# Kernel tuning notes

Measured on AMD Instinct MI355X. Metric: run time of the kernel, lower is better.

## Reference

```python
import jax, jax.numpy as jnp
import numpy as np

H = 12          # heads in the ViT blocks
D = 768         # model dim (hard-coded in the module)
DFF = 3072      # mlp hidden = 4*D
ADIM = 64       # adapter bottleneck dim
L = 32          # num_latents
EPS = 1e-6      # timm ViT LayerNorm eps


def _ln(x, g, b):
    m = jnp.mean(x, axis=-1, keepdims=True)
    v = jnp.var(x, axis=-1, keepdims=True)
    return (x - m) * jax.lax.rsqrt(v + EPS) * g + b


def _quick_gelu(x):
    return x * jax.nn.sigmoid(1.702 * x)


def _sh_attn(q, k, v):
    # single-head attention used by fusion(); scale = C**-0.5 with C = full dim
    C = q.shape[-1]
    a = jax.nn.softmax(jnp.einsum('bnc,bmc->bnm', q, k) * (C ** -0.5), axis=-1)
    return jnp.einsum('bnm,bmc->bnc', a, v)


def _mhsa(x, qkv_w, qkv_b, proj_w, proj_b):
    B, N, C = x.shape
    Dh = C // H
    qkv = (x @ qkv_w.T + qkv_b).reshape(B, N, 3, H, Dh).transpose(2, 0, 3, 1, 4)
    q, k, v = qkv[0], qkv[1], qkv[2]                       # [B,H,N,Dh]
    a = jax.nn.softmax(jnp.einsum('bhnd,bhmd->bhnm', q, k) * (Dh ** -0.5), axis=-1)
    o = jnp.einsum('bhnm,bhmd->bhnd', a, v).transpose(0, 2, 1, 3).reshape(B, N, C)
    return o @ proj_w.T + proj_b


def _stream(t, ln1_g, ln1_b, qkv_w, qkv_b, proj_w, proj_b,
            ln2_g, ln2_b, fc1_w, fc1_b, fc2_w, fc2_b,
            down_w, down_b, up_w, up_b, scale):
    t = t + _mhsa(_ln(t, ln1_g, ln1_b), qkv_w, qkv_b, proj_w, proj_b)
    h = _ln(t, ln2_g, ln2_b)
    mlp = jax.nn.gelu(h @ fc1_w.T + fc1_b, approximate=False) @ fc2_w.T + fc2_b
    adapter = (_quick_gelu(h @ down_w.T + down_b) @ up_w.T + up_b) * scale
    return t + mlp + adapter


def setup_inputs() -> dict:
    key = jax.random.key(0)
    ks = iter(jax.random.split(key, 64))
    f32 = jnp.float32
    def rn(shape, std=0.02):
        return (jax.random.normal(next(ks), shape, dtype=f32) * std)
    inp = {
        'x': jax.random.normal(next(ks), (16, 512, 768), dtype=f32),
        'y': jax.random.normal(next(ks), (16, 196, 768), dtype=f32),
        'latents': rn((1, L, D)),
        'scale_a': jnp.full((1,), 0.5, f32),
        'scale_v': jnp.full((1,), 0.5, f32),
    }
    for p in ('spec', 'rgb'):
        inp.update({
            f'{p}_ln1_g': jnp.ones((D,), f32), f'{p}_ln1_b': jnp.zeros((D,), f32),
            f'{p}_qkv_w': rn((3 * D, D)), f'{p}_qkv_b': jnp.zeros((3 * D,), f32),
            f'{p}_proj_w': rn((D, D)), f'{p}_proj_b': jnp.zeros((D,), f32),
            f'{p}_ln2_g': jnp.ones((D,), f32), f'{p}_ln2_b': jnp.zeros((D,), f32),
            f'{p}_fc1_w': rn((DFF, D)), f'{p}_fc1_b': jnp.zeros((DFF,), f32),
            f'{p}_fc2_w': rn((D, DFF)), f'{p}_fc2_b': jnp.zeros((D,), f32),
            f'{p}_down_w': rn((ADIM, D)), f'{p}_down_b': jnp.zeros((ADIM,), f32),
            f'{p}_up_w': rn((D, ADIM)), f'{p}_up_b': jnp.zeros((D,), f32),
            f'{p}_scale': jnp.ones((1,), f32),
        })
    return inp


def reference(x, y, latents, scale_a, scale_v,
              spec_ln1_g, spec_ln1_b, spec_qkv_w, spec_qkv_b, spec_proj_w, spec_proj_b,
              spec_ln2_g, spec_ln2_b, spec_fc1_w, spec_fc1_b, spec_fc2_w, spec_fc2_b,
              spec_down_w, spec_down_b, spec_up_w, spec_up_b, spec_scale,
              rgb_ln1_g, rgb_ln1_b, rgb_qkv_w, rgb_qkv_b, rgb_proj_w, rgb_proj_b,
              rgb_ln2_g, rgb_ln2_b, rgb_fc1_w, rgb_fc1_b, rgb_fc2_w, rgb_fc2_b,
              rgb_down_w, rgb_down_b, rgb_up_w, rgb_up_b, rgb_scale):
    B = x.shape[0]
    # --- fusion via latent bottleneck (single-head attention) ---
    concat_ = jnp.concatenate((x, y), axis=1)                 # [B, Na+Nv, D]
    lat = jnp.broadcast_to(latents, (B, L, D))
    fused = _sh_attn(lat, concat_, concat_)                   # [B, L, D]
    x = x + scale_a * _sh_attn(x, fused, fused)
    y = y + scale_v * _sh_attn(y, fused, fused)
    # --- per-stream transformer block + adapter (dropout = eval/identity) ---
    x = _stream(x, spec_ln1_g, spec_ln1_b, spec_qkv_w, spec_qkv_b, spec_proj_w, spec_proj_b,
                spec_ln2_g, spec_ln2_b, spec_fc1_w, spec_fc1_b, spec_fc2_w, spec_fc2_b,
                spec_down_w, spec_down_b, spec_up_w, spec_up_b, spec_scale)
    y = _stream(y, rgb_ln1_g, rgb_ln1_b, rgb_qkv_w, rgb_qkv_b, rgb_proj_w, rgb_proj_b,
                rgb_ln2_g, rgb_ln2_b, rgb_fc1_w, rgb_fc1_b, rgb_fc2_w, rgb_fc2_b,
                rgb_down_w, rgb_down_b, rgb_up_w, rgb_up_b, rgb_scale)
    return (x, y)
```

## Files before the change

kernel.cpp:

```cpp
#include <hip/hip_runtime.h>
#include <hip/hip_bf16.h>


#define H_HEADS 12
#define DMODEL 768
#define DFF 3072
#define ADIM 64
#define NLAT 32
#define BATCH 16
#define NA 512
#define NV 196
#define NTOT 708
#define MCAT (BATCH * NTOT)

typedef __hip_bfloat16 bf16;
using bf16x8 = __attribute__((ext_vector_type(8))) short;
using f32x4  = __attribute__((ext_vector_type(4))) float;

static __device__ __forceinline__ float bf2f(bf16 v) { return __bfloat162float(v); }
static __device__ __forceinline__ float bflo(unsigned u) { return __uint_as_float(u << 16); }
static __device__ __forceinline__ float ld1(const float* p) { return *p; }
static __device__ __forceinline__ float ld1(const bf16* p) { return bf2f(*p); }
static __device__ __forceinline__ unsigned short f2bf_bits(float v) {
    unsigned u = __float_as_uint(v);
    return (unsigned short)((u + 0x7fffu + ((u >> 16) & 1u)) >> 16);
}

#define GLD_LDS16(gp, lp) __builtin_amdgcn_global_load_lds( \
    (const __attribute__((address_space(1))) void*)(gp), \
    (__attribute__((address_space(3))) void*)(lp), 16, 0, 0)

__global__ void detect_dtype_kernel(const unsigned short* __restrict__ x, int* __restrict__ flag)
{
    if (threadIdx.x == 0 && blockIdx.x == 0) {
        int big = 0;
        for (int i = 0; i < 2048; i++) {
            unsigned e = (x[i] >> 7) & 0xFF;
            if (e >= 0x90) big++;
        }
        flag[0] = (big > 16) ? 1 : 0;
        flag[1] = 0;
    }
}

template<typename TIn>
static __device__ __forceinline__ void pack_body(
    const TIn* __restrict__ x, const TIn* __restrict__ y, const TIn* __restrict__ lat,
    bf16* __restrict__ Cc, bf16* __restrict__ Lb)
{
    const int r = blockIdx.x, tid = threadIdx.x;
    const TIn* src;
    bf16* dst;
    if (r < MCAT) {
        const int b = r / NTOT, n = r - b * NTOT;
        src = (n < NA) ? x + ((size_t)(b * NA + n)) * DMODEL
                       : y + ((size_t)(b * NV + (n - NA))) * DMODEL;
        dst = Cc + (size_t)r * DMODEL;
    } else {
        src = lat + (size_t)(r - MCAT) * DMODEL;
        dst = Lb + (size_t)(r - MCAT) * DMODEL;
    }
    dst[tid]       = __float2bfloat16(ld1(src + tid));
    dst[tid + 256] = __float2bfloat16(ld1(src + tid + 256));
    dst[tid + 512] = __float2bfloat16(ld1(src + tid + 512));
}

__global__ __launch_bounds__(256)
void pack_concat_kernel(const int* __restrict__ flag, const void* x, const void* y,
                        const void* lat, bf16* __restrict__ Cc, bf16* __restrict__ Lb)
{
    if (flag[0]) pack_body<float>((const float*)x, (const float*)y, (const float*)lat, Cc, Lb);
    else         pack_body<bf16>((const bf16*)x, (const bf16*)y, (const bf16*)lat, Cc, Lb);
}

__global__ __launch_bounds__(64)
void fusion_softmax_kernel(const float* __restrict__ scores, float* __restrict__ P)
{
    const int b = blockIdx.x >> 5, l = blockIdx.x & 31, lane = threadIdx.x;
    const float* sp = scores + (size_t)b * NTOT * NLAT + l;
    float v[12];
    float mx = -1e30f;
    #pragma unroll
    for (int i = 0; i < 12; i++) {
        const int n = lane + i * 64;
        v[i] = (n < NTOT) ? sp[(size_t)n * NLAT] * 0.03608439182435161f : -1e30f;
        mx = fmaxf(mx, v[i]);
    }
    #pragma unroll
    for (int off = 32; off; off >>= 1) mx = fmaxf(mx, __shfl_xor(mx, off));
    float den = 0.f;
    #pragma unroll
    for (int i = 0; i < 12; i++) { v[i] = __expf(v[i] - mx); den += v[i]; }
    #pragma unroll
    for (int off = 32; off; off >>= 1) den += __shfl_xor(den, off);
    const float inv = 1.0f / den;
    float* op = P + ((size_t)b * NLAT + l) * 768;
    #pragma unroll
    for (int i = 0; i < 12; i++) {
        const int n = lane + i * 64;
        op[n] = (n < NTOT) ? v[i] * inv : 0.f;
    }
}

__global__ __launch_bounds__(256)
void fusion_wsum_kernel(const bf16* __restrict__ Cc, const float* __restrict__ P,
                        bf16* __restrict__ fused)
{
    const int b = blockIdx.y, d0 = blockIdx.x * 128;
    const int tid = threadIdx.x;
    const int lg = tid >> 5, dg = tid & 31;
    const int l0 = lg * 4;

    __shared__ float Ct[64][132];
    __shared__ float Ps[32][68];

    float acc[4][4] = {};

    for (int nc = 0; nc < 12; nc++) {
        const int n0 = nc * 64;
        __syncthreads();
        #pragma unroll
        for (int it = 0; it < 8; it++) {
            const int idx = it * 1024 + tid * 4;
            const int r = idx >> 7, c = idx & 127;
            const int gn = n0 + r;
            float4 v = make_float4(0.f, 0.f, 0.f, 0.f);
            if (gn < NTOT) {
                const ushort4 u = *(const ushort4*)(Cc + ((size_t)(b * NTOT + gn)) * DMODEL + d0 + c);
                v = make_float4(bflo(u.x), bflo(u.y), bflo(u.z), bflo(u.w));
            }
            Ct[r][c] = v.x; Ct[r][c + 1] = v.y; Ct[r][c + 2] = v.z; Ct[r][c + 3] = v.w;
        }
        {
            const int l = tid >> 3, off = (tid & 7) * 8;
            const float* pp = P + ((size_t)b * NLAT + l) * 768 + n0 + off;
            const float4 p0 = *(const float4*)pp;
            const float4 p1 = *(const float4*)(pp + 4);
            Ps[l][off] = p0.x; Ps[l][off + 1] = p0.y; Ps[l][off + 2] = p0.z; Ps[l][off + 3] = p0.w;
            Ps[l][off + 4] = p1.x; Ps[l][off + 5] = p1.y; Ps[l][off + 6] = p1.z; Ps[l][off + 7] = p1.w;
        }
        __syncthreads();

        for (int n = 0; n < 64; n++) {
            const float4 v = *(const float4*)&Ct[n][dg * 4];
            #pragma unroll
            for (int i = 0; i < 4; i++) {
                const float p = Ps[l0 + i][n];
                acc[i][0] += p * v.x; acc[i][1] += p * v.y;
                acc[i][2] += p * v.z; acc[i][3] += p * v.w;
            }
        }
    }

    #pragma unroll
    for (int i = 0; i < 4; i++) {
        bf16* op = fused + ((size_t)b * NLAT + l0 + i) * DMODEL + d0 + dg * 4;
        #pragma unroll
        for (int j = 0; j < 4; j++) op[j] = __float2bfloat16(acc[i][j]);
    }
}

template<typename TIn>
static __device__ __forceinline__ void attend_fused_body(
    const TIn* __restrict__ t, const bf16* __restrict__ fused,
    const TIn* __restrict__ scale_p, bf16* __restrict__ out, int Npb)
{
    const int tid = threadIdx.x;
    const int gid = blockIdx.x;
    const int b = gid / Npb;
    const TIn* row = t + (size_t)gid * DMODEL;
    const bf16* fb = fused + (size_t)b * NLAT * DMODEL;

    __shared__ float q[DMODEL];
    __shared__ float p[NLAT];

    for (int d = tid; d < DMODEL; d += 256) q[d] = ld1(row + d);
    __syncthreads();

    const int g = tid >> 3, li = tid & 7;
    float s = 0.f;
    const bf16* fr = fb + (size_t)g * DMODEL;
    for (int d = li; d < DMODEL; d += 8) s += q[d] * bf2f(fr[d]);
    s += __shfl_xor(s, 1); s += __shfl_xor(s, 2); s += __shfl_xor(s, 4);
    if (li == 0) p[g] = s * 0.03608439182435161f;
    __syncthreads();

    float mx = -1e30f;
    #pragma unroll
    for (int l = 0; l < NLAT; l++) mx = fmaxf(mx, p[l]);
    float w[NLAT];
    float den = 0.f;
    #pragma unroll
    for (int l = 0; l < NLAT; l++) { w[l] = __expf(p[l] - mx); den += w[l]; }
    const float sA = ld1(scale_p) / den;

    float a0 = 0.f, a1 = 0.f, a2 = 0.f;
    #pragma unroll
    for (int l = 0; l < NLAT; l++) {
        const bf16* fv = fb + (size_t)l * DMODEL;
        a0 += w[l] * bf2f(fv[tid]);
        a1 += w[l] * bf2f(fv[tid + 256]);
        a2 += w[l] * bf2f(fv[tid + 512]);
    }
    bf16* o = out + (size_t)gid * DMODEL;
    o[tid]       = __float2bfloat16(q[tid]       + sA * a0);
    o[tid + 256] = __float2bfloat16(q[tid + 256] + sA * a1);
    o[tid + 512] = __float2bfloat16(q[tid + 512] + sA * a2);
}

__global__ __launch_bounds__(256)
void attend_fused_kernel(const int* __restrict__ flag, const void* t, const bf16* __restrict__ fused,
                         const void* scale_p, bf16* __restrict__ out, int Npb)
{
    if (flag[0]) attend_fused_body<float>((const float*)t, fused, (const float*)scale_p, out, Npb);
    else         attend_fused_body<bf16>((const bf16*)t, fused, (const bf16*)scale_p, out, Npb);
}

template<typename TW>
static __device__ __forceinline__ void ln_body(
    const bf16* __restrict__ in, const TW* __restrict__ g,
    const TW* __restrict__ bta, bf16* __restrict__ out)
{
    const int tid = threadIdx.x;
    const bf16* p = in + (size_t)blockIdx.x * DMODEL;
    const float v0 = bf2f(p[tid]), v1 = bf2f(p[tid + 256]), v2 = bf2f(p[tid + 512]);
    float s = v0 + v1 + v2;
    float sq = v0 * v0 + v1 * v1 + v2 * v2;
    #pragma unroll
    for (int off = 32; off; off >>= 1) { s += __shfl_xor(s, off); sq += __shfl_xor(sq, off); }
    __shared__ float rs[4], rq[4];
    if ((tid & 63) == 0) { rs[tid >> 6] = s; rq[tid >> 6] = sq; }
    __syncthreads();
    s = rs[0] + rs[1] + rs[2] + rs[3];
    sq = rq[0] + rq[1] + rq[2] + rq[3];
    const float mean = s * (1.0f / DMODEL);
    const float var = sq * (1.0f / DMODEL) - mean * mean;
    const float r = rsqrtf(var + 1e-6f);
    bf16* o = out + (size_t)blockIdx.x * DMODEL;
    o[tid]       = __float2bfloat16((v0 - mean) * r * ld1(g + tid)       + ld1(bta + tid));
    o[tid + 256] = __float2bfloat16((v1 - mean) * r * ld1(g + tid + 256) + ld1(bta + tid + 256));
    o[tid + 512] = __float2bfloat16((v2 - mean) * r * ld1(g + tid + 512) + ld1(bta + tid + 512));
}

__global__ __launch_bounds__(256)
void ln_kernel(const int* __restrict__ flag, const bf16* __restrict__ in,
               const void* g, const void* b, bf16* __restrict__ out)
{
    if (flag[0]) ln_body<float>(in, (const float*)g, (const float*)b, out);
    else         ln_body<bf16>(in, (const bf16*)g, (const bf16*)b, out);
}

__global__ __launch_bounds__(256)
void flash_attn_kernel(const bf16* __restrict__ qkv, bf16* __restrict__ o, int Npb)
{
    const int tid = threadIdx.x;
    const int wv = tid >> 6, lane = tid & 63;
    const int l15 = lane & 15, q4 = lane >> 4;
    const int qt = blockIdx.x, h = blockIdx.y, bb = blockIdx.z;
    const int nkv = (Npb + 63) >> 6;
    const size_t tokbase = (size_t)bb * Npb;

    __shared__ __align__(16) short Ks[64 * 64];
    __shared__ __align__(16) short Vt[64 * 64];
    __shared__ __align__(16) short Ps[4][16 * 64];

    const int qr = min(qt * 64 + wv * 16 + l15, Npb - 1);
    const bf16* qp = qkv + (tokbase + qr) * 2304 + h * 64;
    const bf16x8 qf0 = *(const bf16x8*)(const void*)(qp + q4 * 8);
    const bf16x8 qf1 = *(const bf16x8*)(const void*)(qp + 32 + q4 * 8);

    f32x4 Oa[4] = {};
    float mrow[4], lrow[4];
    #pragma unroll
    for (int i = 0; i < 4; i++) { mrow[i] = -1e30f; lrow[i] = 0.f; }

    for (int kv = 0; kv < nkv; kv++) {
        const int kv0 = kv * 64;
        __syncthreads();
        #pragma unroll
        for (int inst = 0; inst < 2; inst++) {
            const int s = inst * 256 + tid;
            const int row = s >> 3, pos = s & 7;
            const int c = pos ^ (row & 7);
            const int krc = min(kv0 + row, Npb - 1);
            GLD_LDS16(qkv + (tokbase + krc) * 2304 + DMODEL + h * 64 + c * 8, &Ks[s * 8]);
        }
        {
            const int r = tid >> 2;
            const int f0 = (tid & 3) * 16;
            const int krc = min(kv0 + r, Npb - 1);
            const short* vp = (const short*)(qkv + (tokbase + krc) * 2304 + 2 * DMODEL + h * 64 + f0);
            short vb[16];
            *(uint4*)&vb[0] = *(const uint4*)vp;
            *(uint4*)&vb[8] = *(const uint4*)(vp + 8);
            const int chunk = r >> 3, r7 = r & 7;
            #pragma unroll
            for (int j = 0; j < 16; j++) {
                const int feat = f0 + j;
                Vt[feat * 64 + (chunk ^ (feat & 7)) * 8 + r7] = vb[j];
            }
        }
        __syncthreads();

        f32x4 s4[4] = {};
        #pragma unroll
        for (int kk = 0; kk < 2; kk++) {
            const bf16x8 qf = kk ? qf1 : qf0;
            const int c = kk * 4 + q4;
            #pragma unroll
            for (int g = 0; g < 4; g++) {
                const int r = g * 16 + l15;
                const bf16x8 kf = *(const bf16x8*)(const void*)&Ks[r * 64 + (c ^ (r & 7)) * 8];
                s4[g] = __builtin_amdgcn_mfma_f32_16x16x32_bf16(qf, kf, s4[g], 0, 0, 0);
            }
        }
        float tmax[4];
        #pragma unroll
        for (int i = 0; i < 4; i++) tmax[i] = -1e30f;
        #pragma unroll
        for (int g = 0; g < 4; g++) {
            const bool valid = (kv0 + g * 16 + l15) < Npb;
            #pragma unroll
            for (int i = 0; i < 4; i++) {
                const float v = s4[g][i] * 0.125f;
                s4[g][i] = valid ? v : -1e30f;
                tmax[i] = fmaxf(tmax[i], s4[g][i]);
            }
        }
        #pragma unroll
        for (int off = 1; off < 16; off <<= 1)
            #pragma unroll
            for (int i = 0; i < 4; i++) tmax[i] = fmaxf(tmax[i], __shfl_xor(tmax[i], off));
        float alpha[4], rsum[4];
        #pragma unroll
        for (int i = 0; i < 4; i++) {
            const float mn = fmaxf(mrow[i], tmax[i]);
            alpha[i] = __expf(mrow[i] - mn);
            mrow[i] = mn;
            rsum[i] = 0.f;
        }
        #pragma unroll
        for (int g = 0; g < 4; g++) {
            const int cc = g * 16 + l15;
            const int chunk = cc >> 3;
            #pragma unroll
            for (int i = 0; i < 4; i++) {
                const int r = q4 * 4 + i;
                const float p = __expf(s4[g][i] - mrow[i]);
                rsum[i] += p;
                Ps[wv][r * 64 + (chunk ^ (r & 7)) * 8 + (cc & 7)] = (short)f2bf_bits(p);
            }
        }
        #pragma unroll
        for (int off = 1; off < 16; off <<= 1)
            #pragma unroll
            for (int i = 0; i < 4; i++) rsum[i] += __shfl_xor(rsum[i], off);
        #pragma unroll
        for (int i = 0; i < 4; i++) lrow[i] = lrow[i] * alpha[i] + rsum[i];
        #pragma unroll
        for (int g = 0; g < 4; g++)
            #pragma unroll
            for (int i = 0; i < 4; i++) Oa[g][i] *= alpha[i];

        #pragma unroll
        for (int kk = 0; kk < 2; kk++) {
            const int c = kk * 4 + q4;
            const bf16x8 pf = *(const bf16x8*)(const void*)&Ps[wv][l15 * 64 + (c ^ (l15 & 7)) * 8];
            #pragma unroll
            for (int g = 0; g < 4; g++) {
                const int feat = g * 16 + l15;
                const bf16x8 vf = *(const bf16x8*)(const void*)&Vt[feat * 64 + (c ^ (feat & 7)) * 8];
                Oa[g] = __builtin_amdgcn_mfma_f32_16x16x32_bf16(pf, vf, Oa[g], 0, 0, 0);
            }
        }
    }

    float inv[4];
    #pragma unroll
    for (int i = 0; i < 4; i++) inv[i] = 1.0f / lrow[i];
    #pragma unroll
    for (int g = 0; g < 4; g++) {
        const int colo = h * 64 + g * 16 + l15;
        #pragma unroll
        for (int i = 0; i < 4; i++) {
            const int rowg = qt * 64 + wv * 16 + q4 * 4 + i;
            if (rowg < Npb)
                o[(tokbase + rowg) * DMODEL + colo] = __float2bfloat16(Oa[g][i] * inv[i]);
        }
    }
}

template<typename TW, int ACT, bool RES, bool SCALE>
static __device__ __forceinline__ void gemm_body(
    const bf16* __restrict__ A, const TW* __restrict__ W, const TW* __restrict__ bias,
    const bf16* __restrict__ resid, const TW* __restrict__ scale_p, void* __restrict__ C,
    bool cf32, int row_off, int M, int N, int K, short* As, short* Bs)
{
    const int tid = threadIdx.x;
    const int lane = tid & 63;
    const int wv = tid >> 6;
    const int l15 = lane & 15, q4 = lane >> 4;
    const int m0 = blockIdx.y * 128, n0 = blockIdx.x * 128;
    const int wm = (wv & 1) * 64, wn = (wv >> 1) * 64;

    f32x4 acc[4][4] = {};

    for (int k0 = 0; k0 < K; k0 += 32) {
        __syncthreads();
        #pragma unroll
        for (int inst = 0; inst < 2; inst++) {
            const int s = inst * 256 + tid;
            const int row = s >> 2, pos = s & 3;
            const int c = pos ^ ((row >> 1) & 3);
            const int ra = min(m0 + row, M - 1);
            const int rb = min(n0 + row, N - 1);
            GLD_LDS16(A + (size_t)ra * K + k0 + c * 8, &As[s * 8]);
            if (sizeof(TW) == 2) {
                GLD_LDS16((const bf16*)W + (size_t)rb * K + k0 + c * 8, &Bs[s * 8]);
            } else {
                const float* wp = (const float*)W + (size_t)rb * K + k0 + c * 8;
                const float4 w0 = *(const float4*)wp;
                const float4 w1 = *(const float4*)(wp + 4);
                unsigned short hb[8];
                hb[0] = f2bf_bits(w0.x); hb[1] = f2bf_bits(w0.y);
                hb[2] = f2bf_bits(w0.z); hb[3] = f2bf_bits(w0.w);
                hb[4] = f2bf_bits(w1.x); hb[5] = f2bf_bits(w1.y);
                hb[6] = f2bf_bits(w1.z); hb[7] = f2bf_bits(w1.w);
                *(uint4*)&Bs[s * 8] = *(const uint4*)hb;
            }
        }
        __syncthreads();

        bf16x8 af[4], bfr[4];
        #pragma unroll
        for (int f = 0; f < 4; f++) {
            const int r = wm + f * 16 + l15;
            af[f] = *(const bf16x8*)(const void*)&As[r * 32 + (q4 ^ ((r >> 1) & 3)) * 8];
            const int rn = wn + f * 16 + l15;
            bfr[f] = *(const bf16x8*)(const void*)&Bs[rn * 32 + (q4 ^ ((rn >> 1) & 3)) * 8];
        }
        #pragma unroll
        for (int f = 0; f < 4; f++)
            #pragma unroll
            for (int g = 0; g < 4; g++)
                acc[f][g] = __builtin_amdgcn_mfma_f32_16x16x32_bf16(af[f], bfr[g], acc[f][g], 0, 0, 0);
    }

    const float sc = SCALE ? ld1(scale_p) : 1.0f;
    #pragma unroll
    for (int g = 0; g < 4; g++) {
        const int colg = n0 + wn + g * 16 + l15;
        if (colg >= N) continue;
        const float bv = bias ? ld1(bias + colg) : 0.f;
        #pragma unroll
        for (int f = 0; f < 4; f++) {
            const int rowb = m0 + wm + f * 16 + q4 * 4;
            #pragma unroll
            for (int i = 0; i < 4; i++) {
                const int rowg = rowb + i;
                if (rowg >= M) continue;
                float v = acc[f][g][i] + bv;
                if (ACT == 1) v = 0.5f * v * (1.0f + erff(v * 0.70710678118654752f));
                else if (ACT == 2) v = v / (1.0f + __expf(-1.702f * v));
                if (SCALE) v *= sc;
                const size_t idx = (size_t)rowg * N + colg;
                if (RES) v += bf2f(resid[idx]);
                const size_t sidx = (size_t)(rowg + row_off) * N + colg;
                if (cf32) ((float*)C)[sidx] = v;
                else ((bf16*)C)[sidx] = __float2bfloat16(v);
            }
        }
    }
}

template<int ACT, bool RES, bool SCALE>
__global__ __launch_bounds__(256)
void mfma_gemm_kernel(const int* __restrict__ flag, const bf16* __restrict__ A,
                      const void* __restrict__ W, const void* __restrict__ bias,
                      const bf16* __restrict__ resid, const void* __restrict__ sp,
                      void* __restrict__ C, int out_mode, int row_off, int M, int N, int K)
{
    __shared__ __align__(16) short As[128 * 32];
    __shared__ __align__(16) short Bs[128 * 32];
    const bool cf32 = (out_mode == 2) || (out_mode == 1 && flag[0] != 0);
    if (flag[0])
        gemm_body<float, ACT, RES, SCALE>(A, (const float*)W, (const float*)bias, resid,
                                          (const float*)sp, C, cf32, row_off, M, N, K, As, Bs);
    else
        gemm_body<bf16, ACT, RES, SCALE>(A, (const bf16*)W, (const bf16*)bias, resid,
                                         (const bf16*)sp, C, cf32, row_off, M, N, K, As, Bs);
}

struct SW {
    const void *ln1_g, *ln1_b, *qkv_w, *qkv_b, *proj_w, *proj_b,
               *ln2_g, *ln2_b, *fc1_w, *fc1_b, *fc2_w, *fc2_b,
               *down_w, *down_b, *up_w, *up_b, *scale;
};

static void run_stream(const int* flag, bf16* t0, int M, int Npb, int nb, const SW& w,
                       bf16* h, bf16* big, bf16* ah, void* out, int out_row_off, hipStream_t s)
{
    const dim3 g768((DMODEL + 127) / 128, (M + 127) / 128);
    const dim3 g2304((2304 + 127) / 128, (M + 127) / 128);
    const dim3 g3072((DFF + 127) / 128, (M + 127) / 128);
    const dim3 g64((ADIM + 127) / 128, (M + 127) / 128);

    ln_kernel<<<M, 256, 0, s>>>(flag, t0, w.ln1_g, w.ln1_b, h);
    mfma_gemm_kernel<0, false, false><<<g2304, 256, 0, s>>>(
        flag, h, w.qkv_w, w.qkv_b, nullptr, nullptr, big, 0, 0, M, 2304, DMODEL);
    flash_attn_kernel<<<dim3((Npb + 63) / 64, H_HEADS, nb), 256, 0, s>>>(big, h, Npb);
    mfma_gemm_kernel<0, true, false><<<g768, 256, 0, s>>>(
        flag, h, w.proj_w, w.proj_b, t0, nullptr, t0, 0, 0, M, DMODEL, DMODEL);
    ln_kernel<<<M, 256, 0, s>>>(flag, t0, w.ln2_g, w.ln2_b, h);
    mfma_gemm_kernel<1, false, false><<<g3072, 256, 0, s>>>(
        flag, h, w.fc1_w, w.fc1_b, nullptr, nullptr, big, 0, 0, M, DFF, DMODEL);
    mfma_gemm_kernel<2, false, false><<<g64, 256, 0, s>>>(
        flag, h, w.down_w, w.down_b, nullptr, nullptr, ah, 0, 0, M, ADIM, DMODEL);
    mfma_gemm_kernel<0, true, false><<<g768, 256, 0, s>>>(
        flag, big, w.fc2_w, w.fc2_b, t0, nullptr, t0, 0, 0, M, DMODEL, DFF);
    mfma_gemm_kernel<0, true, true><<<g768, 256, 0, s>>>(
        flag, ah, w.up_w, w.up_b, t0, w.scale, out, 1, out_row_off, M, DMODEL, ADIM);
}

extern "C" void kernel_launch(void* const* d_in, const int* in_sizes, int n_in,
                              void* d_out, int out_size, void* d_ws, size_t ws_size,
                              hipStream_t stream)
{
    SW sw, rw;
    auto fill = [&](SW& s, int base) {
        s.ln1_g = d_in[base + 0];  s.ln1_b = d_in[base + 1];
        s.qkv_w = d_in[base + 2];  s.qkv_b = d_in[base + 3];
        s.proj_w = d_in[base + 4]; s.proj_b = d_in[base + 5];
        s.ln2_g = d_in[base + 6];  s.ln2_b = d_in[base + 7];
        s.fc1_w = d_in[base + 8];  s.fc1_b = d_in[base + 9];
        s.fc2_w = d_in[base + 10]; s.fc2_b = d_in[base + 11];
        s.down_w = d_in[base + 12]; s.down_b = d_in[base + 13];
        s.up_w = d_in[base + 14];  s.up_b = d_in[base + 15];
        s.scale = d_in[base + 16];
    };
    fill(sw, 5);
    fill(rw, 22);

    const int Mx = BATCH * NA;
    const int My = BATCH * NV;

    int* flag = (int*)d_ws;
    char* base = (char*)d_ws + 256;
    bf16* x1 = (bf16*)base;                base += (size_t)Mx * DMODEL * 2;
    bf16* y1 = (bf16*)base;                base += (size_t)My * DMODEL * 2;
    bf16* fused = (bf16*)base;             base += (size_t)BATCH * NLAT * DMODEL * 2;
    char* un = base;

    bf16* Cc = (bf16*)un;
    bf16* Lb = (bf16*)(un + (size_t)MCAT * DMODEL * 2);
    float* scores = (float*)(un + (size_t)(MCAT + 64) * DMODEL * 2);
    float* P = (float*)((char*)scores + (size_t)MCAT * NLAT * 4 + 256);

    const size_t stream_need_big = ((size_t)Mx * DMODEL + (size_t)Mx * DFF + (size_t)Mx * ADIM) * 2;
    const size_t fixed = 256 + ((size_t)Mx * DMODEL + (size_t)My * DMODEL + (size_t)BATCH * NLAT * DMODEL) * 2;
    const bool big_ws = ws_size >= fixed + stream_need_big;
    const int hrows = big_ws ? Mx : My;
    bf16* h  = (bf16*)un;
    bf16* big = h + (size_t)hrows * DMODEL;
    bf16* ah = big + (size_t)hrows * DFF;

    detect_dtype_kernel<<<1, 64, 0, stream>>>((const unsigned short*)d_in[0], flag);

    pack_concat_kernel<<<MCAT + NLAT, 256, 0, stream>>>(flag, d_in[0], d_in[1], d_in[2], Cc, Lb);
    mfma_gemm_kernel<0, false, false><<<dim3(1, (MCAT + 127) / 128), 256, 0, stream>>>(
        flag + 1, Cc, Lb, nullptr, nullptr, nullptr, scores, 2, 0, MCAT, NLAT, DMODEL);
    fusion_softmax_kernel<<<BATCH * NLAT, 64, 0, stream>>>(scores, P);
    fusion_wsum_kernel<<<dim3(DMODEL / 128, BATCH), 256, 0, stream>>>(Cc, P, fused);

    attend_fused_kernel<<<BATCH * NA, 256, 0, stream>>>(flag, d_in[0], fused, d_in[3], x1, NA);
    attend_fused_kernel<<<BATCH * NV, 256, 0, stream>>>(flag, d_in[1], fused, d_in[4], y1, NV);

    if (big_ws) {
        run_stream(flag, x1, Mx, NA, BATCH, sw, h, big, ah, d_out, 0, stream);
    } else {
        const int MCH = 2048;
        for (int c = 0; c < Mx / MCH; c++)
            run_stream(flag, x1 + (size_t)c * MCH * DMODEL, MCH, NA, MCH / NA, sw,
                       h, big, ah, d_out, c * MCH, stream);
    }
    run_stream(flag, y1, My, NV, BATCH, rw, h, big, ah, d_out, Mx, stream);
}
```

Baseline: 1.293 ms.

## Fuse LN1 into attend, merge fc1+down GEMM, widen K-tile, swap grid order

Fuses LayerNorm-1 into the fused-latent attend kernel, which removes one LN launch and a read of the activations per stream. Merges the adapter down-projection into the fc1 GEMM by appending its rows to the weight tile, with a per-column activation choice. The GEMM changes from a K-step of 32 to 64 with a new swizzle, uses 64-row M-tiles for the N=768 GEMMs, and puts the M tiles on grid x padded to a multiple of 8. The flash-attention grid is also reordered. This adds more LDS per block and a branch per column in the fused GEMM epilogue, and the y-stream attend now runs after the x stream so it can reuse the h buffer.

After: 1.349 ms. 1.04x slower.

```diff
diff --git a/kernel.cpp b/kernel.cpp
--- a/kernel.cpp
+++ b/kernel.cpp
@@ -29,6 +29,8 @@
 #define GLD_LDS16(gp, lp) __builtin_amdgcn_global_load_lds( \
     (const __attribute__((address_space(1))) void*)(gp), \
     (__attribute__((address_space(3))) void*)(lp), 16, 0, 0)
+
+static inline int pad8(int v) { return (v + 7) & ~7; }
 
 __global__ void detect_dtype_kernel(const unsigned short* __restrict__ x, int* __restrict__ flag)
 {
@@ -163,7 +165,8 @@
 template<typename TIn>
 static __device__ __forceinline__ void attend_fused_body(
     const TIn* __restrict__ t, const bf16* __restrict__ fused,
-    const TIn* __restrict__ scale_p, bf16* __restrict__ out, int Npb)
+    const TIn* __restrict__ scale_p, const TIn* __restrict__ lng, const TIn* __restrict__ lnb,
+    bf16* __restrict__ out, bf16* __restrict__ hout, int Npb)
 {
     const int tid = threadIdx.x;
     const int gid = blockIdx.x;
@@ -173,6 +176,7 @@
 
     __shared__ float q[DMODEL];
     __shared__ float p[NLAT];
+    __shared__ float rs[4], rq[4];
 
     for (int d = tid; d < DMODEL; d += 256) q[d] = ld1(row + d);
     __syncthreads();
@@ -202,18 +206,42 @@
         a1 += w[l] * bf2f(fv[tid + 256]);
         a2 += w[l] * bf2f(fv[tid + 512]);
     }
+    const float t0v = q[tid] + sA * a0;
+    const float t1v = q[tid + 256] + sA * a1;
+    const float t2v = q[tid + 512] + sA * a2;
     bf16* o = out + (size_t)gid * DMODEL;
-    o[tid]       = __float2bfloat16(q[tid]       + sA * a0);
-    o[tid + 256] = __float2bfloat16(q[tid + 256] + sA * a1);
-    o[tid + 512] = __float2bfloat16(q[tid + 512] + sA * a2);
+    o[tid]       = __float2bfloat16(t0v);
+    o[tid + 256] = __float2bfloat16(t1v);
+    o[tid + 512] = __float2bfloat16(t2v);
+
+    if (hout) {
+        float ss = t0v + t1v + t2v;
+        float sq = t0v * t0v + t1v * t1v + t2v * t2v;
+        #pragma unroll
+        for (int off = 32; off; off >>= 1) { ss += __shfl_xor(ss, off); sq += __shfl_xor(sq, off); }
+        if ((tid & 63) == 0) { rs[tid >> 6] = ss; rq[tid >> 6] = sq; }
+        __syncthreads();
+        ss = rs[0] + rs[1] + rs[2] + rs[3];
+        sq = rq[0] + rq[1] + rq[2] + rq[3];
+        const float mean = ss * (1.0f / DMODEL);
+        const float var = sq * (1.0f / DMODEL) - mean * mean;
+        const float r = rsqrtf(var + 1e-6f);
+        bf16* ho = hout + (size_t)gid * DMODEL;
+        ho[tid]       = __float2bfloat16((t0v - mean) * r * ld1(lng + tid)       + ld1(lnb + tid));
+        ho[tid + 256] = __float2bfloat16((t1v - mean) * r * ld1(lng + tid + 256) + ld1(lnb + tid + 256));
+        ho[tid + 512] = __float2bfloat16((t2v - mean) * r * ld1(lng + tid + 512) + ld1(lnb + tid + 512));
+    }
 }
 
 __global__ __launch_bounds__(256)
 void attend_fused_kernel(const int* __restrict__ flag, const void* t, const bf16* __restrict__ fused,
-                         const void* scale_p, bf16* __restrict__ out, int Npb)
-{
-    if (flag[0]) attend_fused_body<float>((const float*)t, fused, (const float*)scale_p, out, Npb);
-    else         attend_fused_body<bf16>((const bf16*)t, fused, (const bf16*)scale_p, out, Npb);
+                         const void* scale_p, const void* lng, const void* lnb,
+                         bf16* __restrict__ out, bf16* __restrict__ hout, int Npb)
+{
+    if (flag[0]) attend_fused_body<float>((const float*)t, fused, (const float*)scale_p,
+                                          (const float*)lng, (const float*)lnb, out, hout, Npb);
+    else         attend_fused_body<bf16>((const bf16*)t, fused, (const bf16*)scale_p,
+                                         (const bf16*)lng, (const bf16*)lnb, out, hout, Npb);
 }
 
 template<typename TW>
@@ -256,7 +284,8 @@
     const int tid = threadIdx.x;
     const int wv = tid >> 6, lane = tid & 63;
     const int l15 = lane & 15, q4 = lane >> 4;
-    const int qt = blockIdx.x, h = blockIdx.y, bb = blockIdx.z;
+    const int h = blockIdx.x % H_HEADS, bb = blockIdx.x / H_HEADS;
+    const int qt = blockIdx.y;
     const int nkv = (Npb + 63) >> 6;
     const size_t tokbase = (size_t)bb * Npb;
 
@@ -390,68 +419,89 @@
     }
 }
 
-template<typename TW, int ACT, bool RES, bool SCALE>
+template<int TM, int ACT, bool RES, bool SCALE, bool FD, typename TW>
 static __device__ __forceinline__ void gemm_body(
-    const bf16* __restrict__ A, const TW* __restrict__ W, const TW* __restrict__ bias,
-    const bf16* __restrict__ resid, const TW* __restrict__ scale_p, void* __restrict__ C,
+    const bf16* __restrict__ A, const TW* __restrict__ W, const TW* __restrict__ Wd,
+    const TW* __restrict__ bias, const TW* __restrict__ biasd,
+    const bf16* __restrict__ resid, const TW* __restrict__ scale_p,
+    void* __restrict__ C, bf16* __restrict__ Cd,
     bool cf32, int row_off, int M, int N, int K, short* As, short* Bs)
 {
     const int tid = threadIdx.x;
     const int lane = tid & 63;
     const int wv = tid >> 6;
     const int l15 = lane & 15, q4 = lane >> 4;
-    const int m0 = blockIdx.y * 128, n0 = blockIdx.x * 128;
-    const int wm = (wv & 1) * 64, wn = (wv >> 1) * 64;
-
-    f32x4 acc[4][4] = {};
-
-    for (int k0 = 0; k0 < K; k0 += 32) {
+    const int m0 = blockIdx.x * TM, n0 = blockIdx.y * 128;
+    const int N1 = FD ? N - ADIM : N;
+    constexpr int NF = (TM == 128) ? 4 : 2;
+    const int wm = (TM == 128) ? (wv & 1) * 64 : 0;
+    const int wn = (TM == 128) ? (wv >> 1) * 64 : wv * 32;
+
+    f32x4 acc[4][NF] = {};
+
+    for (int k0 = 0; k0 < K; k0 += 64) {
         __syncthreads();
-        #pragma unroll
-        for (int inst = 0; inst < 2; inst++) {
-            const int s = inst * 256 + tid;
-            const int row = s >> 2, pos = s & 3;
-            const int c = pos ^ ((row >> 1) & 3);
+        constexpr int AIT = TM * 8 / 256;
+        #pragma unroll
+        for (int it = 0; it < AIT; it++) {
+            const int i = it * 256 + tid;
+            const int row = i >> 3, pos = i & 7;
+            const int c = pos ^ (row & 7);
             const int ra = min(m0 + row, M - 1);
+            GLD_LDS16(A + (size_t)ra * K + k0 + c * 8, &As[i * 8]);
+        }
+        #pragma unroll
+        for (int it = 0; it < 4; it++) {
+            const int i = it * 256 + tid;
+            const int row = i >> 3, pos = i & 7;
+            const int c = pos ^ (row & 7);
             const int rb = min(n0 + row, N - 1);
-            GLD_LDS16(A + (size_t)ra * K + k0 + c * 8, &As[s * 8]);
-            if (sizeof(TW) == 2) {
-                GLD_LDS16((const bf16*)W + (size_t)rb * K + k0 + c * 8, &Bs[s * 8]);
+            const TW* wp = (FD && rb >= N1) ? Wd + (size_t)(rb - N1) * K
+                                            : W + (size_t)rb * K;
+            if constexpr (sizeof(TW) == 2) {
+                GLD_LDS16(wp + k0 + c * 8, &Bs[i * 8]);
             } else {
-                const float* wp = (const float*)W + (size_t)rb * K + k0 + c * 8;
-                const float4 w0 = *(const float4*)wp;
-                const float4 w1 = *(const float4*)(wp + 4);
+                const float* fp = (const float*)wp + k0 + c * 8;
+                const float4 w0 = *(const float4*)fp;
+                const float4 w1 = *(const float4*)(fp + 4);
                 unsigned short hb[8];
                 hb[0] = f2bf_bits(w0.x); hb[1] = f2bf_bits(w0.y);
                 hb[2] = f2bf_bits(w0.z); hb[3] = f2bf_bits(w0.w);
                 hb[4] = f2bf_bits(w1.x); hb[5] = f2bf_bits(w1.y);
                 hb[6] = f2bf_bits(w1.z); hb[7] = f2bf_bits(w1.w);
-                *(uint4*)&Bs[s * 8] = *(const uint4*)hb;
+                *(uint4*)&Bs[i * 8] = *(const uint4*)hb;
             }
         }
         __syncthreads();
 
-        bf16x8 af[4], bfr[4];
-        #pragma unroll
-        for (int f = 0; f < 4; f++) {
-            const int r = wm + f * 16 + l15;
-            af[f] = *(const bf16x8*)(const void*)&As[r * 32 + (q4 ^ ((r >> 1) & 3)) * 8];
-            const int rn = wn + f * 16 + l15;
-            bfr[f] = *(const bf16x8*)(const void*)&Bs[rn * 32 + (q4 ^ ((rn >> 1) & 3)) * 8];
-        }
-        #pragma unroll
-        for (int f = 0; f < 4; f++)
-            #pragma unroll
-            for (int g = 0; g < 4; g++)
-                acc[f][g] = __builtin_amdgcn_mfma_f32_16x16x32_bf16(af[f], bfr[g], acc[f][g], 0, 0, 0);
+        #pragma unroll
+        for (int kk = 0; kk < 2; kk++) {
+            bf16x8 af[4], bfr[NF];
+            #pragma unroll
+            for (int f = 0; f < 4; f++) {
+                const int r = wm + f * 16 + l15;
+                af[f] = *(const bf16x8*)(const void*)&As[(r * 8 + ((kk * 4 + q4) ^ (r & 7))) * 8];
+            }
+            #pragma unroll
+            for (int g = 0; g < NF; g++) {
+                const int rn = wn + g * 16 + l15;
+                bfr[g] = *(const bf16x8*)(const void*)&Bs[(rn * 8 + ((kk * 4 + q4) ^ (rn & 7))) * 8];
+            }
+            #pragma unroll
+            for (int f = 0; f < 4; f++)
+                #pragma unroll
+                for (int g = 0; g < NF; g++)
+                    acc[f][g] = __builtin_amdgcn_mfma_f32_16x16x32_bf16(af[f], bfr[g], acc[f][g], 0, 0, 0);
+        }
     }
 
     const float sc = SCALE ? ld1(scale_p) : 1.0f;
     #pragma unroll
-    for (int g = 0; g < 4; g++) {
+    for (int g = 0; g < NF; g++) {
         const int colg = n0 + wn + g * 16 + l15;
         if (colg >= N) continue;
-        const float bv = bias ? ld1(bias + colg) : 0.f;
+        const bool isdown = FD && (colg >= N1);
+        const float bv = bias ? (isdown ? ld1(biasd + colg - N1) : ld1(bias + colg)) : 0.f;
         #pragma unroll
         for (int f = 0; f < 4; f++) {
             const int rowb = m0 + wm + f * 16 + q4 * 4;
@@ -460,35 +510,46 @@
                 const int rowg = rowb + i;
                 if (rowg >= M) continue;
                 float v = acc[f][g][i] + bv;
-                if (ACT == 1) v = 0.5f * v * (1.0f + erff(v * 0.70710678118654752f));
+                if (FD) {
+                    if (isdown) v = v / (1.0f + __expf(-1.702f * v));
+                    else v = 0.5f * v * (1.0f + erff(v * 0.70710678118654752f));
+                } else if (ACT == 1) v = 0.5f * v * (1.0f + erff(v * 0.70710678118654752f));
                 else if (ACT == 2) v = v / (1.0f + __expf(-1.702f * v));
                 if (SCALE) v *= sc;
-                const size_t idx = (size_t)rowg * N + colg;
-                if (RES) v += bf2f(resid[idx]);
-                const size_t sidx = (size_t)(rowg + row_off) * N + colg;
-                if (cf32) ((float*)C)[sidx] = v;
-                else ((bf16*)C)[sidx] = __float2bfloat16(v);
-            }
-        }
-    }
-}
-
-template<int ACT, bool RES, bool SCALE>
+                if (RES) v += bf2f(resid[(size_t)rowg * N + colg]);
+                if (FD && isdown) {
+                    Cd[(size_t)rowg * ADIM + (colg - N1)] = __float2bfloat16(v);
+                } else {
+                    const size_t sidx = (size_t)(rowg + row_off) * N1 + colg;
+                    if (cf32) ((float*)C)[sidx] = v;
+                    else ((bf16*)C)[sidx] = __float2bfloat16(v);
+                }
+            }
+        }
+    }
+}
+
+template<int TM, int ACT, bool RES, bool SCALE, bool FD>
 __global__ __launch_bounds__(256)
 void mfma_gemm_kernel(const int* __restrict__ flag, const bf16* __restrict__ A,
-                      const void* __restrict__ W, const void* __restrict__ bias,
+                      const void* __restrict__ W, const void* __restrict__ Wd,
+                      const void* __restrict__ bias, const void* __restrict__ biasd,
                       const bf16* __restrict__ resid, const void* __restrict__ sp,
-                      void* __restrict__ C, int out_mode, int row_off, int M, int N, int K)
-{
-    __shared__ __align__(16) short As[128 * 32];
-    __shared__ __align__(16) short Bs[128 * 32];
+                      void* __restrict__ C, bf16* __restrict__ Cd,
+                      int out_mode, int row_off, int M, int N, int K)
+{
+    __shared__ __align__(16) short As[TM * 64];
+    __shared__ __align__(16) short Bs[128 * 64];
+    if (blockIdx.x * TM >= M) return;
     const bool cf32 = (out_mode == 2) || (out_mode == 1 && flag[0] != 0);
     if (flag[0])
-        gemm_body<float, ACT, RES, SCALE>(A, (const float*)W, (const float*)bias, resid,
-                                          (const float*)sp, C, cf32, row_off, M, N, K, As, Bs);
+        gemm_body<TM, ACT, RES, SCALE, FD, float>(A, (const float*)W, (const float*)Wd,
+            (const float*)bias, (const float*)biasd, resid, (const float*)sp, C, Cd,
+            cf32, row_off, M, N, K, As, Bs);
     else
-        gemm_body<bf16, ACT, RES, SCALE>(A, (const bf16*)W, (const bf16*)bias, resid,
-                                         (const bf16*)sp, C, cf32, row_off, M, N, K, As, Bs);
+        gemm_body<TM, ACT, RES, SCALE, FD, bf16>(A, (const bf16*)W, (const bf16*)Wd,
+            (const bf16*)bias, (const bf16*)biasd, resid, (const bf16*)sp, C, Cd,
+            cf32, row_off, M, N, K, As, Bs);
 }
 
 struct SW {
@@ -498,28 +559,33 @@
 };
 
 static void run_stream(const int* flag, bf16* t0, int M, int Npb, int nb, const SW& w,
-                       bf16* h, bf16* big, bf16* ah, void* out, int out_row_off, hipStream_t s)
-{
-    const dim3 g768((DMODEL + 127) / 128, (M + 127) / 128);
-    const dim3 g2304((2304 + 127) / 128, (M + 127) / 128);
-    const dim3 g3072((DFF + 127) / 128, (M + 127) / 128);
-    const dim3 g64((ADIM + 127) / 128, (M + 127) / 128);
-
-    ln_kernel<<<M, 256, 0, s>>>(flag, t0, w.ln1_g, w.ln1_b, h);
-    mfma_gemm_kernel<0, false, false><<<g2304, 256, 0, s>>>(
-        flag, h, w.qkv_w, w.qkv_b, nullptr, nullptr, big, 0, 0, M, 2304, DMODEL);
-    flash_attn_kernel<<<dim3((Npb + 63) / 64, H_HEADS, nb), 256, 0, s>>>(big, h, Npb);
-    mfma_gemm_kernel<0, true, false><<<g768, 256, 0, s>>>(
-        flag, h, w.proj_w, w.proj_b, t0, nullptr, t0, 0, 0, M, DMODEL, DMODEL);
+                       bf16* h, bf16* big, bf16* ah, void* out, int out_row_off,
+                       bool skip_ln1, hipStream_t s)
+{
+    const int mt128 = pad8((M + 127) / 128);
+    const int mt64  = pad8((M + 63) / 64);
+    const dim3 gqkv(mt128, 18);
+    const dim3 gfc1(mt128, 25);
+    const dim3 g768(mt64, 6);
+
+    if (!skip_ln1) ln_kernel<<<M, 256, 0, s>>>(flag, t0, w.ln1_g, w.ln1_b, h);
+    mfma_gemm_kernel<128, 0, false, false, false><<<gqkv, 256, 0, s>>>(
+        flag, h, w.qkv_w, nullptr, w.qkv_b, nullptr, nullptr, nullptr, big, nullptr,
+        0, 0, M, 2304, DMODEL);
+    flash_attn_kernel<<<dim3(nb * H_HEADS, (Npb + 63) / 64), 256, 0, s>>>(big, h, Npb);
+    mfma_gemm_kernel<64, 0, true, false, false><<<g768, 256, 0, s>>>(
+        flag, h, w.proj_w, nullptr, w.proj_b, nullptr, t0, nullptr, t0, nullptr,
+        0, 0, M, DMODEL, DMODEL);
     ln_kernel<<<M, 256, 0, s>>>(flag, t0, w.ln2_g, w.ln2_b, h);
-    mfma_gemm_kernel<1, false, false><<<g3072, 256, 0, s>>>(
-        flag, h, w.fc1_w, w.fc1_b, nullptr, nullptr, big, 0, 0, M, DFF, DMODEL);
-    mfma_gemm_kernel<2, false, false><<<g64, 256, 0, s>>>(
-        flag, h, w.down_w, w.down_b, nullptr, nullptr, ah, 0, 0, M, ADIM, DMODEL);
-    mfma_gemm_kernel<0, true, false><<<g768, 256, 0, s>>>(
-        flag, big, w.fc2_w, w.fc2_b, t0, nullptr, t0, 0, 0, M, DMODEL, DFF);
-    mfma_gemm_kernel<0, true, true><<<g768, 256, 0, s>>>(
-        flag, ah, w.up_w, w.up_b, t0, w.scale, out, 1, out_row_off, M, DMODEL, ADIM);
+    mfma_gemm_kernel<128, 1, false, false, true><<<gfc1, 256, 0, s>>>(
+        flag, h, w.fc1_w, w.down_w, w.fc1_b, w.down_b, nullptr, nullptr, big, ah,
+        0, 0, M, DFF + ADIM, DMODEL);
+    mfma_gemm_kernel<64, 0, true, false, false><<<g768, 256, 0, s>>>(
+        flag, big, w.fc2_w, nullptr, w.fc2_b, nullptr, t0, nullptr, t0, nullptr,
+        0, 0, M, DMODEL, DFF);
+    mfma_gemm_kernel<64, 0, true, true, false><<<g768, 256, 0, s>>>(
+        flag, ah, w.up_w, nullptr, w.up_b, nullptr, t0, w.scale, out, nullptr,
+        1, out_row_off, M, DMODEL, ADIM);
 }
 
 extern "C" void kernel_launch(void* const* d_in, const int* in_sizes, int n_in,
@@ -567,21 +633,24 @@
     detect_dtype_kernel<<<1, 64, 0, stream>>>((const unsigned short*)d_in[0], flag);
 
     pack_concat_kernel<<<MCAT + NLAT, 256, 0, stream>>>(flag, d_in[0], d_in[1], d_in[2], Cc, Lb);
-    mfma_gemm_kernel<0, false, false><<<dim3(1, (MCAT + 127) / 128), 256, 0, stream>>>(
-        flag + 1, Cc, Lb, nullptr, nullptr, nullptr, scores, 2, 0, MCAT, NLAT, DMODEL);
+    mfma_gemm_kernel<128, 0, false, false, false><<<dim3(pad8((MCAT + 127) / 128), 1), 256, 0, stream>>>(
+        flag + 1, Cc, Lb, nullptr, nullptr, nullptr, nullptr, nullptr, scores, nullptr,
+        2, 0, MCAT, NLAT, DMODEL);
     fusion_softmax_kernel<<<BATCH * NLAT, 64, 0, stream>>>(scores, P);
     fusion_wsum_kernel<<<dim3(DMODEL / 128, BATCH), 256, 0, stream>>>(Cc, P, fused);
 
-    attend_fused_kernel<<<BATCH * NA, 256, 0, stream>>>(flag, d_in[0], fused, d_in[3], x1, NA);
-    attend_fused_kernel<<<BATCH * NV, 256, 0, stream>>>(flag, d_in[1], fused, d_in[4], y1, NV);
-
+    attend_fused_kernel<<<BATCH * NA, 256, 0, stream>>>(
+        flag, d_in[0], fused, d_in[3], sw.ln1_g, sw.ln1_b, x1, big_ws ? h : nullptr, NA);
     if (big_ws) {
-        run_stream(flag, x1, Mx, NA, BATCH, sw, h, big, ah, d_out, 0, stream);
+        run_stream(flag, x1, Mx, NA, BATCH, sw, h, big, ah, d_out, 0, true, stream);
     } else {
         const int MCH = 2048;
         for (int c = 0; c < Mx / MCH; c++)
             run_stream(flag, x1 + (size_t)c * MCH * DMODEL, MCH, NA, MCH / NA, sw,
-                       h, big, ah, d_out, c * MCH, stream);
-    }
-    run_stream(flag, y1, My, NV, BATCH, rw, h, big, ah, d_out, Mx, stream);
-}
+                       h, big, ah, d_out, c * MCH, false, stream);
+    }
+
+    attend_fused_kernel<<<BATCH * NV, 256, 0, stream>>>(
+        flag, d_in[1], fused, d_in[4], rw.ln1_g, rw.ln1_b, y1, h, NV);
+    run_stream(flag, y1, My, NV, BATCH, rw, h, big, ah, d_out, Mx, true, stream);
+}
```
